# Kernel tuning notes

Hardware: AMD Instinct MI355X
Metric: run time of the kernel (lower is better)

Reference implementation:

```python
import jax, jax.numpy as jnp
import numpy as np

BASE = 10000.0

def positional_encoding(seq_len, dim, dtype=jnp.float32):
    # standard sinusoidal PE: pe[p, 2i] = sin(p / BASE^(2i/dim)), pe[p, 2i+1] = cos(...)
    pos = jnp.arange(seq_len, dtype=dtype)[:, None]            # [S,1]
    idx = jnp.arange(0, dim, 2, dtype=dtype)[None, :]          # [1,dim/2]
    ang = pos / jnp.power(BASE, idx / dim)                     # [S,dim/2]
    pe = jnp.zeros((seq_len, dim), dtype=dtype)
    pe = pe.at[:, 0::2].set(jnp.sin(ang)).at[:, 1::2].set(jnp.cos(ang))
    return pe

def setup_inputs() -> dict:
    key = jax.random.key(0)
    ks = jax.random.split(key, 5)
    B, S, H, D = 16, 2048, 128, 64
    x = jax.random.normal(ks[0], (B, S, H), dtype=jnp.float32)
    Wq = jax.random.normal(ks[1], (H, D), dtype=jnp.float32) * (H ** -0.5)
    Wk = jax.random.normal(ks[2], (H, D), dtype=jnp.float32) * (H ** -0.5)
    Wv = jax.random.normal(ks[3], (H, D), dtype=jnp.float32) * (H ** -0.5)
    Wf = jax.random.normal(ks[4], (D, 1), dtype=jnp.float32) * (D ** -0.5)
    bf = jnp.zeros((1,), dtype=jnp.float32)
    return {"x": x, "Wq": Wq, "Wk": Wk, "Wv": Wv, "Wf": Wf, "bf": bf}

def reference(x, Wq, Wk, Wv, Wf, bf):
    B, S, H = x.shape
    xp = x + positional_encoding(S, H, x.dtype)[None]          # add PE, broadcast over batch
    Q = jnp.einsum('bsh,hd->bsd', xp, Wq)
    K = jnp.einsum('bsh,hd->bsd', xp, Wk)
    V = jnp.einsum('bsh,hd->bsd', xp, Wv)
    D = K.shape[-1]
    scores = jnp.einsum('bqd,bkd->bqk', Q, K) / jnp.sqrt(jnp.asarray(D, x.dtype))
    # NOTE: softmax over dim=1 (the QUERY axis), per the original nn.Softmax(dim=1)
    attn = jax.nn.softmax(scores, axis=1)                      # [B,S,S]
    z = jnp.einsum('bqk,bkd->bqd', attn, V)                    # [B,S,D]
    out = (jnp.einsum('bsd,do->bso', z, Wf) + bf).squeeze(-1)  # [B,S]
    return out
```

## Files before the change

kernel.cpp:

```cpp
#include <hip/hip_runtime.h>
#include <hip/hip_bf16.h>
#include <math.h>

#define BATCH 16
#define SEQ   2048
#define HID   128
#define DIM   64
#define WTP   136

typedef __attribute__((ext_vector_type(8))) short bf16x8;
typedef __attribute__((ext_vector_type(4))) float f32x4;

#define QSCALE 0.18033688011112042f
#define C0_PE  0.07195578314043169f

static __device__ __forceinline__ ushort f2bf(float f) {
    union { float f; unsigned u; } v; v.f = f;
    unsigned r = v.u + 0x7FFFu + ((v.u >> 16) & 1u);
    return (ushort)(r >> 16);
}

static __device__ __forceinline__ float fast_exp2(float x) {
#if __has_builtin(__builtin_amdgcn_exp2f)
    return __builtin_amdgcn_exp2f(x);
#else
    return exp2f(x);
#endif
}

__global__ __launch_bounds__(256) void k_qkv(
    const float* __restrict__ x, const float* __restrict__ Wq,
    const float* __restrict__ Wk, const float* __restrict__ Wv,
    const float* __restrict__ Wf, ushort* __restrict__ Qb,
    ushort* __restrict__ Kb, float* __restrict__ vf)
{
    __shared__ ushort Wt[128 * WTP];
    __shared__ float  wvl[HID];

    const int tid  = threadIdx.x;
    const int wave = tid >> 6;
    const int lane = tid & 63;
    const int quad = lane >> 4;
    const int col  = lane & 15;

    if (tid < HID) {
        float s = 0.f;
        #pragma unroll 8
        for (int d = 0; d < DIM; ++d) s += Wv[tid * DIM + d] * Wf[d];
        wvl[tid] = s;
    }
    for (int i = tid; i < 128 * 128; i += 256) {
        int k = i >> 7, oc = i & 127;
        float v = (oc < 64) ? Wq[k * DIM + oc] * QSCALE : Wk[k * DIM + (oc - 64)];
        Wt[oc * WTP + k] = f2bf(v);
    }
    __syncthreads();

    const int rowbase = blockIdx.x * 64 + wave * 16;
    const int grow = rowbase + col;
    const float pos = (float)(grow & (SEQ - 1));

    bf16x8 af[4];
    float vpart = 0.f;
    #pragma unroll
    for (int c = 0; c < 4; ++c) {
        const float* xp = x + (size_t)grow * HID + quad * 8 + c * 32;
        float4 v0 = *(const float4*)(xp);
        float4 v1 = *(const float4*)(xp + 4);
        float t[8] = {v0.x, v0.y, v0.z, v0.w, v1.x, v1.y, v1.z, v1.w};
        #pragma unroll
        for (int jp = 0; jp < 4; ++jp) {
            int h = quad * 8 + c * 32 + jp * 2;
            float ang = pos * __expf(-(float)h * C0_PE);
            t[jp * 2]     += __sinf(ang);
            t[jp * 2 + 1] += __cosf(ang);
        }
        const float* wp = wvl + quad * 8 + c * 32;
        vpart += t[0] * wp[0] + t[1] * wp[1] + t[2] * wp[2] + t[3] * wp[3] +
                 t[4] * wp[4] + t[5] * wp[5] + t[6] * wp[6] + t[7] * wp[7];
        short* ap = (short*)&af[c];
        #pragma unroll
        for (int j = 0; j < 8; ++j) ap[j] = (short)f2bf(t[j]);
    }

    vpart += __shfl_xor(vpart, 16);
    vpart += __shfl_xor(vpart, 32);
    if (quad == 0) vf[grow] = vpart;

    #pragma unroll
    for (int t = 0; t < 8; ++t) {
        const ushort* wrow = Wt + (size_t)(t * 16 + col) * WTP + quad * 8;
        f32x4 acc = {0.f, 0.f, 0.f, 0.f};
        #pragma unroll
        for (int c = 0; c < 4; ++c) {
            bf16x8 wfr = *(const bf16x8*)(wrow + c * 32);
            acc = __builtin_amdgcn_mfma_f32_16x16x32_bf16(wfr, af[c], acc, 0, 0, 0);
        }
        ushort4 o = {f2bf(acc.x), f2bf(acc.y), f2bf(acc.z), f2bf(acc.w)};
        ushort* dst = (t < 4) ? Qb : Kb;
        *(ushort4*)&dst[(size_t)grow * DIM + (t & 3) * 16 + quad * 4] = o;
    }
}

__global__ __launch_bounds__(512) void k_attn(
    const ushort* __restrict__ Qb, const ushort* __restrict__ Kb,
    const float* __restrict__ vf, const float* __restrict__ bfp,
    float* __restrict__ outp)
{
    const int b    = blockIdx.y;
    const int k0   = blockIdx.x * 64;
    const int tid  = threadIdx.x;
    const int wave = tid >> 6;
    const int lane = tid & 63;
    const int quad = lane >> 4;
    const int col  = lane & 15;

    __shared__ float sl[8][64];
    __shared__ float wcol[64];

    bf16x8 kf[4][2];
    {
        const ushort* Kbase = Kb + ((size_t)(b * SEQ + k0)) * DIM;
        #pragma unroll
        for (int t = 0; t < 4; ++t)
            #pragma unroll
            for (int c = 0; c < 2; ++c)
                kf[t][c] = *(const bf16x8*)(Kbase + (size_t)(t * 16 + col) * DIM + quad * 8 + c * 32);
    }

    const ushort* Qstart = Qb + ((size_t)(b * SEQ + wave * 256 + col)) * DIM + quad * 8;

    float l[4][4] = {};
    {
        const ushort* Qrow = Qstart;
        for (int qi = 0; qi < 16; ++qi) {
            bf16x8 q0 = *(const bf16x8*)(Qrow);
            bf16x8 q1 = *(const bf16x8*)(Qrow + 32);
            Qrow += 16 * DIM;
            #pragma unroll
            for (int t = 0; t < 4; ++t) {
                f32x4 acc = {0.f, 0.f, 0.f, 0.f};
                acc = __builtin_amdgcn_mfma_f32_16x16x32_bf16(kf[t][0], q0, acc, 0, 0, 0);
                acc = __builtin_amdgcn_mfma_f32_16x16x32_bf16(kf[t][1], q1, acc, 0, 0, 0);
                #pragma unroll
                for (int r = 0; r < 4; ++r)
                    l[t][r] += fast_exp2(acc[r]);
            }
        }
    }
    #pragma unroll
    for (int t = 0; t < 4; ++t)
        #pragma unroll
        for (int r = 0; r < 4; ++r) {
            float v = l[t][r];
            v += __shfl_xor(v, 1); v += __shfl_xor(v, 2);
            v += __shfl_xor(v, 4); v += __shfl_xor(v, 8);
            l[t][r] = v;
        }
    if (col == 0) {
        #pragma unroll
        for (int t = 0; t < 4; ++t)
            #pragma unroll
            for (int r = 0; r < 4; ++r)
                sl[wave][t * 16 + quad * 4 + r] = l[t][r];
    }
    __syncthreads();
    if (tid < 64) {
        float ll = 0.f;
        #pragma unroll
        for (int w = 0; w < 8; ++w) ll += sl[w][tid];
        wcol[tid] = vf[(size_t)b * SEQ + k0 + tid] / ll;
    }
    __syncthreads();

    float wreg[4][4];
    #pragma unroll
    for (int t = 0; t < 4; ++t)
        #pragma unroll
        for (int r = 0; r < 4; ++r)
            wreg[t][r] = wcol[t * 16 + quad * 4 + r];

    const float bias = bfp[0] * (1.0f / (SEQ / 64));
    float* outb = outp + (size_t)b * SEQ;
    {
        const ushort* Qrow = Qstart;
        for (int qi = 0; qi < 16; ++qi) {
            bf16x8 q0 = *(const bf16x8*)(Qrow);
            bf16x8 q1 = *(const bf16x8*)(Qrow + 32);
            Qrow += 16 * DIM;
            float rs = 0.f;
            #pragma unroll
            for (int t = 0; t < 4; ++t) {
                f32x4 acc = {0.f, 0.f, 0.f, 0.f};
                acc = __builtin_amdgcn_mfma_f32_16x16x32_bf16(kf[t][0], q0, acc, 0, 0, 0);
                acc = __builtin_amdgcn_mfma_f32_16x16x32_bf16(kf[t][1], q1, acc, 0, 0, 0);
                #pragma unroll
                for (int r = 0; r < 4; ++r)
                    rs += fast_exp2(acc[r]) * wreg[t][r];
            }
            rs += __shfl_xor(rs, 16);
            rs += __shfl_xor(rs, 32);
            if (quad == 0)
                atomicAdd(&outb[wave * 256 + qi * 16 + col], rs + bias);
        }
    }
}

extern "C" void kernel_launch(void* const* d_in, const int* in_sizes, int n_in,
                              void* d_out, int out_size, void* d_ws, size_t ws_size,
                              hipStream_t stream) {
    (void)in_sizes; (void)n_in; (void)ws_size;
    const float* x  = (const float*)d_in[0];
    const float* Wq = (const float*)d_in[1];
    const float* Wk = (const float*)d_in[2];
    const float* Wv = (const float*)d_in[3];
    const float* Wf = (const float*)d_in[4];
    const float* bf = (const float*)d_in[5];
    float* outp = (float*)d_out;

    float*  vf = (float*)d_ws;
    ushort* Qb = (ushort*)(vf + (size_t)BATCH * SEQ);
    ushort* Kb = Qb + (size_t)BATCH * SEQ * DIM;

    hipMemsetAsync(d_out, 0, (size_t)out_size * sizeof(float), stream);
    k_qkv<<<BATCH * SEQ / 64, 256, 0, stream>>>(x, Wq, Wk, Wv, Wf, Qb, Kb, vf);
    k_attn<<<dim3(SEQ / 64, BATCH), 512, 0, stream>>>(Qb, Kb, vf, bf, outp);
}
```

Before: 139.5 us.

## Split attention into stats and output kernels with query-chunked grid, precompute PE and weights

The fused attention kernel becomes two kernels. k_stats accumulates the column softmax denominators over query chunks using atomics into a global buffer, and k_out applies them. Each kernel uses a 4x larger grid of 256-thread blocks, which raises parallelism across CUs. The positional encoding table and the transposed bf16 Q/K weights are now precomputed once by separate kernels instead of per block in shared memory, which removes the per-block transcendental and weight-staging work. The cost is extra launches, a memset, atomics and K fragments that are reloaded in both passes.

Result: slower. 158.3 us (+13.5%).

```diff
diff --git a/kernel.cpp b/kernel.cpp
--- a/kernel.cpp
+++ b/kernel.cpp
@@ -6,7 +6,6 @@
 #define SEQ   2048
 #define HID   128
 #define DIM   64
-#define WTP   136
 
 typedef __attribute__((ext_vector_type(8))) short bf16x8;
 typedef __attribute__((ext_vector_type(4))) float f32x4;
@@ -28,56 +27,62 @@
 #endif
 }
 
+__global__ __launch_bounds__(256) void k_pe(float* __restrict__ pet) {
+    int i = blockIdx.x * 256 + threadIdx.x;
+    int pos = i >> 6, hp = i & 63;
+    float ang = (float)pos * __expf(-(float)(2 * hp) * C0_PE);
+    pet[pos * HID + 2 * hp]     = __sinf(ang);
+    pet[pos * HID + 2 * hp + 1] = __cosf(ang);
+}
+
+__global__ void k_prep(const float* __restrict__ Wq, const float* __restrict__ Wk,
+                       const float* __restrict__ Wv, const float* __restrict__ Wf,
+                       ushort* __restrict__ Wt, float* __restrict__ wvf) {
+    const int tid = threadIdx.x;
+    if (tid < HID) {
+        float s = 0.f;
+        #pragma unroll 8
+        for (int d = 0; d < DIM; ++d) s += Wv[tid * DIM + d] * Wf[d];
+        wvf[tid] = s;
+    }
+    for (int i = tid; i < 128 * 128; i += 256) {
+        int col = i >> 7, k = i & 127;
+        float v = (col < 64) ? Wq[k * DIM + col] * QSCALE : Wk[k * DIM + (col - 64)];
+        Wt[i] = f2bf(v);
+    }
+}
+
 __global__ __launch_bounds__(256) void k_qkv(
-    const float* __restrict__ x, const float* __restrict__ Wq,
-    const float* __restrict__ Wk, const float* __restrict__ Wv,
-    const float* __restrict__ Wf, ushort* __restrict__ Qb,
-    ushort* __restrict__ Kb, float* __restrict__ vf)
+    const float* __restrict__ x, const float* __restrict__ pet,
+    const ushort* __restrict__ Wt, const float* __restrict__ wvf,
+    ushort* __restrict__ Qb, ushort* __restrict__ Kb, float* __restrict__ vf)
 {
-    __shared__ ushort Wt[128 * WTP];
-    __shared__ float  wvl[HID];
-
     const int tid  = threadIdx.x;
     const int wave = tid >> 6;
     const int lane = tid & 63;
     const int quad = lane >> 4;
     const int col  = lane & 15;
-
-    if (tid < HID) {
-        float s = 0.f;
-        #pragma unroll 8
-        for (int d = 0; d < DIM; ++d) s += Wv[tid * DIM + d] * Wf[d];
-        wvl[tid] = s;
-    }
-    for (int i = tid; i < 128 * 128; i += 256) {
-        int k = i >> 7, oc = i & 127;
-        float v = (oc < 64) ? Wq[k * DIM + oc] * QSCALE : Wk[k * DIM + (oc - 64)];
-        Wt[oc * WTP + k] = f2bf(v);
-    }
-    __syncthreads();
-
     const int rowbase = blockIdx.x * 64 + wave * 16;
     const int grow = rowbase + col;
-    const float pos = (float)(grow & (SEQ - 1));
+    const int pos  = grow & (SEQ - 1);
 
     bf16x8 af[4];
     float vpart = 0.f;
     #pragma unroll
     for (int c = 0; c < 4; ++c) {
-        const float* xp = x + (size_t)grow * HID + quad * 8 + c * 32;
+        const float* xp = x   + (size_t)grow * HID + quad * 8 + c * 32;
+        const float* pp = pet + (size_t)pos  * HID + quad * 8 + c * 32;
         float4 v0 = *(const float4*)(xp);
         float4 v1 = *(const float4*)(xp + 4);
-        float t[8] = {v0.x, v0.y, v0.z, v0.w, v1.x, v1.y, v1.z, v1.w};
-        #pragma unroll
-        for (int jp = 0; jp < 4; ++jp) {
-            int h = quad * 8 + c * 32 + jp * 2;
-            float ang = pos * __expf(-(float)h * C0_PE);
-            t[jp * 2]     += __sinf(ang);
-            t[jp * 2 + 1] += __cosf(ang);
-        }
-        const float* wp = wvl + quad * 8 + c * 32;
-        vpart += t[0] * wp[0] + t[1] * wp[1] + t[2] * wp[2] + t[3] * wp[3] +
-                 t[4] * wp[4] + t[5] * wp[5] + t[6] * wp[6] + t[7] * wp[7];
+        float4 p0 = *(const float4*)(pp);
+        float4 p1 = *(const float4*)(pp + 4);
+        float t[8] = {v0.x + p0.x, v0.y + p0.y, v0.z + p0.z, v0.w + p0.w,
+                      v1.x + p1.x, v1.y + p1.y, v1.z + p1.z, v1.w + p1.w};
+        const float* wp = wvf + quad * 8 + c * 32;
+        float4 w0 = *(const float4*)(wp);
+        float4 w1 = *(const float4*)(wp + 4);
+        vpart += t[0] * w0.x + t[1] * w0.y + t[2] * w0.z + t[3] * w0.w +
+                 t[4] * w1.x + t[5] * w1.y + t[6] * w1.z + t[7] * w1.w;
         short* ap = (short*)&af[c];
         #pragma unroll
         for (int j = 0; j < 8; ++j) ap[j] = (short)f2bf(t[j]);
@@ -89,7 +94,7 @@
 
     #pragma unroll
     for (int t = 0; t < 8; ++t) {
-        const ushort* wrow = Wt + (size_t)(t * 16 + col) * WTP + quad * 8;
+        const ushort* wrow = Wt + (size_t)(t * 16 + col) * 128 + quad * 8;
         f32x4 acc = {0.f, 0.f, 0.f, 0.f};
         #pragma unroll
         for (int c = 0; c < 4; ++c) {
@@ -102,21 +107,21 @@
     }
 }
 
-__global__ __launch_bounds__(512) void k_attn(
+__global__ __launch_bounds__(256) void k_stats(
     const ushort* __restrict__ Qb, const ushort* __restrict__ Kb,
-    const float* __restrict__ vf, const float* __restrict__ bfp,
-    float* __restrict__ outp)
+    float* __restrict__ lb)
 {
-    const int b    = blockIdx.y;
-    const int k0   = blockIdx.x * 64;
+    const int kt   = blockIdx.x;
+    const int qc   = blockIdx.y;
+    const int b    = blockIdx.z;
+    const int k0   = kt * 64;
     const int tid  = threadIdx.x;
     const int wave = tid >> 6;
     const int lane = tid & 63;
     const int quad = lane >> 4;
     const int col  = lane & 15;
 
-    __shared__ float sl[8][64];
-    __shared__ float wcol[64];
+    __shared__ float sl[4][64];
 
     bf16x8 kf[4][2];
     {
@@ -128,26 +133,23 @@
                 kf[t][c] = *(const bf16x8*)(Kbase + (size_t)(t * 16 + col) * DIM + quad * 8 + c * 32);
     }
 
-    const ushort* Qstart = Qb + ((size_t)(b * SEQ + wave * 256 + col)) * DIM + quad * 8;
-
     float l[4][4] = {};
-    {
-        const ushort* Qrow = Qstart;
-        for (int qi = 0; qi < 16; ++qi) {
-            bf16x8 q0 = *(const bf16x8*)(Qrow);
-            bf16x8 q1 = *(const bf16x8*)(Qrow + 32);
-            Qrow += 16 * DIM;
-            #pragma unroll
-            for (int t = 0; t < 4; ++t) {
-                f32x4 acc = {0.f, 0.f, 0.f, 0.f};
-                acc = __builtin_amdgcn_mfma_f32_16x16x32_bf16(kf[t][0], q0, acc, 0, 0, 0);
-                acc = __builtin_amdgcn_mfma_f32_16x16x32_bf16(kf[t][1], q1, acc, 0, 0, 0);
-                #pragma unroll
-                for (int r = 0; r < 4; ++r)
-                    l[t][r] += fast_exp2(acc[r]);
-            }
-        }
-    }
+    const ushort* Qrow = Qb + ((size_t)(b * SEQ + qc * 512 + wave * 128 + col)) * DIM + quad * 8;
+    for (int qi = 0; qi < 8; ++qi) {
+        bf16x8 q0 = *(const bf16x8*)(Qrow);
+        bf16x8 q1 = *(const bf16x8*)(Qrow + 32);
+        Qrow += 16 * DIM;
+        #pragma unroll
+        for (int t = 0; t < 4; ++t) {
+            f32x4 acc = {0.f, 0.f, 0.f, 0.f};
+            acc = __builtin_amdgcn_mfma_f32_16x16x32_bf16(kf[t][0], q0, acc, 0, 0, 0);
+            acc = __builtin_amdgcn_mfma_f32_16x16x32_bf16(kf[t][1], q1, acc, 0, 0, 0);
+            #pragma unroll
+            for (int r = 0; r < 4; ++r)
+                l[t][r] += fast_exp2(acc[r]);
+        }
+    }
+
     #pragma unroll
     for (int t = 0; t < 4; ++t)
         #pragma unroll
@@ -166,10 +168,41 @@
     }
     __syncthreads();
     if (tid < 64) {
-        float ll = 0.f;
-        #pragma unroll
-        for (int w = 0; w < 8; ++w) ll += sl[w][tid];
-        wcol[tid] = vf[(size_t)b * SEQ + k0 + tid] / ll;
+        float s = sl[0][tid] + sl[1][tid] + sl[2][tid] + sl[3][tid];
+        atomicAdd(&lb[(size_t)b * SEQ + k0 + tid], s);
+    }
+}
+
+__global__ __launch_bounds__(256) void k_out(
+    const ushort* __restrict__ Qb, const ushort* __restrict__ Kb,
+    const float* __restrict__ vf, const float* __restrict__ lb,
+    const float* __restrict__ bfp, float* __restrict__ outp)
+{
+    const int kt   = blockIdx.x;
+    const int qc   = blockIdx.y;
+    const int b    = blockIdx.z;
+    const int k0   = kt * 64;
+    const int tid  = threadIdx.x;
+    const int wave = tid >> 6;
+    const int lane = tid & 63;
+    const int quad = lane >> 4;
+    const int col  = lane & 15;
+
+    __shared__ float wcol[64];
+
+    if (tid < 64) {
+        size_t g = (size_t)b * SEQ + k0 + tid;
+        wcol[tid] = vf[g] / lb[g];
+    }
+
+    bf16x8 kf[4][2];
+    {
+        const ushort* Kbase = Kb + ((size_t)(b * SEQ + k0)) * DIM;
+        #pragma unroll
+        for (int t = 0; t < 4; ++t)
+            #pragma unroll
+            for (int c = 0; c < 2; ++c)
+                kf[t][c] = *(const bf16x8*)(Kbase + (size_t)(t * 16 + col) * DIM + quad * 8 + c * 32);
     }
     __syncthreads();
 
@@ -182,27 +215,27 @@
 
     const float bias = bfp[0] * (1.0f / (SEQ / 64));
     float* outb = outp + (size_t)b * SEQ;
-    {
-        const ushort* Qrow = Qstart;
-        for (int qi = 0; qi < 16; ++qi) {
-            bf16x8 q0 = *(const bf16x8*)(Qrow);
-            bf16x8 q1 = *(const bf16x8*)(Qrow + 32);
-            Qrow += 16 * DIM;
-            float rs = 0.f;
-            #pragma unroll
-            for (int t = 0; t < 4; ++t) {
-                f32x4 acc = {0.f, 0.f, 0.f, 0.f};
-                acc = __builtin_amdgcn_mfma_f32_16x16x32_bf16(kf[t][0], q0, acc, 0, 0, 0);
-                acc = __builtin_amdgcn_mfma_f32_16x16x32_bf16(kf[t][1], q1, acc, 0, 0, 0);
-                #pragma unroll
-                for (int r = 0; r < 4; ++r)
-                    rs += fast_exp2(acc[r]) * wreg[t][r];
-            }
-            rs += __shfl_xor(rs, 16);
-            rs += __shfl_xor(rs, 32);
-            if (quad == 0)
-                atomicAdd(&outb[wave * 256 + qi * 16 + col], rs + bias);
-        }
+    const int qbase = qc * 512 + wave * 128;
+    const ushort* Qrow = Qb + ((size_t)(b * SEQ + qbase + col)) * DIM + quad * 8;
+
+    for (int qi = 0; qi < 8; ++qi) {
+        bf16x8 q0 = *(const bf16x8*)(Qrow);
+        bf16x8 q1 = *(const bf16x8*)(Qrow + 32);
+        Qrow += 16 * DIM;
+        float rs = 0.f;
+        #pragma unroll
+        for (int t = 0; t < 4; ++t) {
+            f32x4 acc = {0.f, 0.f, 0.f, 0.f};
+            acc = __builtin_amdgcn_mfma_f32_16x16x32_bf16(kf[t][0], q0, acc, 0, 0, 0);
+            acc = __builtin_amdgcn_mfma_f32_16x16x32_bf16(kf[t][1], q1, acc, 0, 0, 0);
+            #pragma unroll
+            for (int r = 0; r < 4; ++r)
+                rs += fast_exp2(acc[r]) * wreg[t][r];
+        }
+        rs += __shfl_xor(rs, 16);
+        rs += __shfl_xor(rs, 32);
+        if (quad == 0)
+            atomicAdd(&outb[qbase + qi * 16 + col], rs + bias);
     }
 }
 
@@ -218,11 +251,19 @@
     const float* bf = (const float*)d_in[5];
     float* outp = (float*)d_out;
 
-    float*  vf = (float*)d_ws;
-    ushort* Qb = (ushort*)(vf + (size_t)BATCH * SEQ);
-    ushort* Kb = Qb + (size_t)BATCH * SEQ * DIM;
+    float*  wvf = (float*)d_ws;
+    float*  vf  = wvf + 256;
+    float*  lb  = vf + (size_t)BATCH * SEQ;
+    float*  pet = lb + (size_t)BATCH * SEQ;
+    ushort* Wt  = (ushort*)(pet + (size_t)SEQ * HID);
+    ushort* Qb  = Wt + 128 * 128;
+    ushort* Kb  = Qb + (size_t)BATCH * SEQ * DIM;
 
     hipMemsetAsync(d_out, 0, (size_t)out_size * sizeof(float), stream);
-    k_qkv<<<BATCH * SEQ / 64, 256, 0, stream>>>(x, Wq, Wk, Wv, Wf, Qb, Kb, vf);
-    k_attn<<<dim3(SEQ / 64, BATCH), 512, 0, stream>>>(Qb, Kb, vf, bf, outp);
-}
+    hipMemsetAsync(lb, 0, (size_t)BATCH * SEQ * sizeof(float), stream);
+    k_pe<<<SEQ * (HID / 2) / 256, 256, 0, stream>>>(pet);
+    k_prep<<<1, 256, 0, stream>>>(Wq, Wk, Wv, Wf, Wt, wvf);
+    k_qkv<<<BATCH * SEQ / 64, 256, 0, stream>>>(x, pet, Wt, wvf, Qb, Kb, vf);
+    k_stats<<<dim3(SEQ / 64, 4, BATCH), 256, 0, stream>>>(Qb, Kb, lb);
+    k_out<<<dim3(SEQ / 64, 4, BATCH), 256, 0, stream>>>(Qb, Kb, vf, lb, bf, outp);
+}
```

## Precompute positional encoding and weight prep in a separate kernel

Applied to the files above, without the earlier changes.

Adds a prep kernel that computes the sinusoidal PE table once per sequence position and, in its last block, the transposed bf16 Q/K weight matrix and the Wv·Wf vector. The QKV kernel then reads these from global memory instead of recomputing sin/cos/exp per batch element and rebuilding the weight tile in LDS in every block. It also stages x+PE through shared memory with coalesced loads and splits Q and K across 8 waves. The cost is an extra launch, extra global traffic for the PE table and weights, and a serial weight-transpose done by a single block.

Result: no change. 141.4 us (+1.4%).

```diff
diff --git a/kernel.cpp b/kernel.cpp
--- a/kernel.cpp
+++ b/kernel.cpp
@@ -6,7 +6,7 @@
 #define SEQ   2048
 #define HID   128
 #define DIM   64
-#define WTP   136
+#define XSP   136
 
 typedef __attribute__((ext_vector_type(8))) short bf16x8;
 typedef __attribute__((ext_vector_type(4))) float f32x4;
@@ -28,68 +28,90 @@
 #endif
 }
 
-__global__ __launch_bounds__(256) void k_qkv(
-    const float* __restrict__ x, const float* __restrict__ Wq,
-    const float* __restrict__ Wk, const float* __restrict__ Wv,
-    const float* __restrict__ Wf, ushort* __restrict__ Qb,
-    ushort* __restrict__ Kb, float* __restrict__ vf)
+__global__ __launch_bounds__(256) void k_peprep(
+    const float* __restrict__ Wq, const float* __restrict__ Wk,
+    const float* __restrict__ Wv, const float* __restrict__ Wf,
+    float* __restrict__ pet, ushort* __restrict__ Wt, float* __restrict__ wvf)
 {
-    __shared__ ushort Wt[128 * WTP];
-    __shared__ float  wvl[HID];
-
-    const int tid  = threadIdx.x;
+    const int tid = threadIdx.x;
+    int i = blockIdx.x * 256 + tid;
+    int pos = i >> 6, hp = i & 63;
+    float ang = (float)pos * __expf(-(float)(2 * hp) * C0_PE);
+    pet[pos * HID + 2 * hp]     = __sinf(ang);
+    pet[pos * HID + 2 * hp + 1] = __cosf(ang);
+
+    if (blockIdx.x == gridDim.x - 1) {
+        if (tid < HID) {
+            float s = 0.f;
+            #pragma unroll 8
+            for (int d = 0; d < DIM; ++d) s += Wv[tid * DIM + d] * Wf[d];
+            wvf[tid] = s;
+        }
+        for (int j = tid; j < 128 * 128; j += 256) {
+            int col = j >> 7, k = j & 127;
+            float v = (col < 64) ? Wq[k * DIM + col] * QSCALE : Wk[k * DIM + (col - 64)];
+            Wt[j] = f2bf(v);
+        }
+    }
+}
+
+__global__ __launch_bounds__(512) void k_qkv(
+    const float* __restrict__ x, const float* __restrict__ pet,
+    const ushort* __restrict__ Wt, const float* __restrict__ wvf,
+    ushort* __restrict__ Qb, ushort* __restrict__ Kb, float* __restrict__ vf)
+{
+    __shared__ ushort xs[64 * XSP];
+    __shared__ float  vred[64][9];
+
+    const int tid = threadIdx.x;
+
+    {
+        const int srow = tid >> 3;
+        const int soff = (tid & 7) * 16;
+        const int growS = blockIdx.x * 64 + srow;
+        const int posS  = growS & (SEQ - 1);
+        const float4* x4 = (const float4*)(x   + (size_t)growS * HID + soff);
+        const float4* p4 = (const float4*)(pet + (size_t)posS  * HID + soff);
+        const float4* w4 = (const float4*)(wvf + soff);
+        float vpart = 0.f;
+        #pragma unroll
+        for (int j = 0; j < 4; ++j) {
+            float4 a = x4[j];
+            float4 p = p4[j];
+            float4 w = w4[j];
+            float t0 = a.x + p.x, t1 = a.y + p.y, t2 = a.z + p.z, t3 = a.w + p.w;
+            vpart += t0 * w.x + t1 * w.y + t2 * w.z + t3 * w.w;
+            ushort4 o = {f2bf(t0), f2bf(t1), f2bf(t2), f2bf(t3)};
+            *(ushort4*)&xs[srow * XSP + soff + j * 4] = o;
+        }
+        vred[srow][tid & 7] = vpart;
+    }
+    __syncthreads();
+
+    if (tid < 64) {
+        float s = 0.f;
+        #pragma unroll
+        for (int j = 0; j < 8; ++j) s += vred[tid][j];
+        vf[blockIdx.x * 64 + tid] = s;
+    }
+
     const int wave = tid >> 6;
     const int lane = tid & 63;
     const int quad = lane >> 4;
     const int col  = lane & 15;
-
-    if (tid < HID) {
-        float s = 0.f;
-        #pragma unroll 8
-        for (int d = 0; d < DIM; ++d) s += Wv[tid * DIM + d] * Wf[d];
-        wvl[tid] = s;
-    }
-    for (int i = tid; i < 128 * 128; i += 256) {
-        int k = i >> 7, oc = i & 127;
-        float v = (oc < 64) ? Wq[k * DIM + oc] * QSCALE : Wk[k * DIM + (oc - 64)];
-        Wt[oc * WTP + k] = f2bf(v);
-    }
-    __syncthreads();
-
-    const int rowbase = blockIdx.x * 64 + wave * 16;
-    const int grow = rowbase + col;
-    const float pos = (float)(grow & (SEQ - 1));
+    const int rg   = wave & 3;
+    const int half = wave >> 2;
 
     bf16x8 af[4];
-    float vpart = 0.f;
-    #pragma unroll
-    for (int c = 0; c < 4; ++c) {
-        const float* xp = x + (size_t)grow * HID + quad * 8 + c * 32;
-        float4 v0 = *(const float4*)(xp);
-        float4 v1 = *(const float4*)(xp + 4);
-        float t[8] = {v0.x, v0.y, v0.z, v0.w, v1.x, v1.y, v1.z, v1.w};
-        #pragma unroll
-        for (int jp = 0; jp < 4; ++jp) {
-            int h = quad * 8 + c * 32 + jp * 2;
-            float ang = pos * __expf(-(float)h * C0_PE);
-            t[jp * 2]     += __sinf(ang);
-            t[jp * 2 + 1] += __cosf(ang);
-        }
-        const float* wp = wvl + quad * 8 + c * 32;
-        vpart += t[0] * wp[0] + t[1] * wp[1] + t[2] * wp[2] + t[3] * wp[3] +
-                 t[4] * wp[4] + t[5] * wp[5] + t[6] * wp[6] + t[7] * wp[7];
-        short* ap = (short*)&af[c];
-        #pragma unroll
-        for (int j = 0; j < 8; ++j) ap[j] = (short)f2bf(t[j]);
-    }
-
-    vpart += __shfl_xor(vpart, 16);
-    vpart += __shfl_xor(vpart, 32);
-    if (quad == 0) vf[grow] = vpart;
-
-    #pragma unroll
-    for (int t = 0; t < 8; ++t) {
-        const ushort* wrow = Wt + (size_t)(t * 16 + col) * WTP + quad * 8;
+    #pragma unroll
+    for (int c = 0; c < 4; ++c)
+        af[c] = *(const bf16x8*)&xs[(rg * 16 + col) * XSP + quad * 8 + c * 32];
+
+    const int growW = blockIdx.x * 64 + rg * 16 + col;
+    ushort* dst = half ? Kb : Qb;
+    #pragma unroll
+    for (int t = 0; t < 4; ++t) {
+        const ushort* wrow = Wt + (size_t)((half * 4 + t) * 16 + col) * 128 + quad * 8;
         f32x4 acc = {0.f, 0.f, 0.f, 0.f};
         #pragma unroll
         for (int c = 0; c < 4; ++c) {
@@ -97,8 +119,7 @@
             acc = __builtin_amdgcn_mfma_f32_16x16x32_bf16(wfr, af[c], acc, 0, 0, 0);
         }
         ushort4 o = {f2bf(acc.x), f2bf(acc.y), f2bf(acc.z), f2bf(acc.w)};
-        ushort* dst = (t < 4) ? Qb : Kb;
-        *(ushort4*)&dst[(size_t)grow * DIM + (t & 3) * 16 + quad * 4] = o;
+        *(ushort4*)&dst[(size_t)growW * DIM + t * 16 + quad * 4] = o;
     }
 }
 
@@ -218,11 +239,15 @@
     const float* bf = (const float*)d_in[5];
     float* outp = (float*)d_out;
 
-    float*  vf = (float*)d_ws;
-    ushort* Qb = (ushort*)(vf + (size_t)BATCH * SEQ);
-    ushort* Kb = Qb + (size_t)BATCH * SEQ * DIM;
+    float*  wvf = (float*)d_ws;
+    float*  vf  = wvf + 256;
+    float*  pet = vf + (size_t)BATCH * SEQ;
+    ushort* Wt  = (ushort*)(pet + (size_t)SEQ * HID);
+    ushort* Qb  = Wt + 128 * 128;
+    ushort* Kb  = Qb + (size_t)BATCH * SEQ * DIM;
 
     hipMemsetAsync(d_out, 0, (size_t)out_size * sizeof(float), stream);
-    k_qkv<<<BATCH * SEQ / 64, 256, 0, stream>>>(x, Wq, Wk, Wv, Wf, Qb, Kb, vf);
+    k_peprep<<<SEQ * (HID / 2) / 256, 256, 0, stream>>>(Wq, Wk, Wv, Wf, pet, Wt, wvf);
+    k_qkv<<<BATCH * SEQ / 64, 512, 0, stream>>>(x, pet, Wt, wvf, Qb, Kb, vf);
     k_attn<<<dim3(SEQ / 64, BATCH), 512, 0, stream>>>(Qb, Kb, vf, bf, outp);
 }
```
